# Kernel optimization log

Measured on AMD Instinct MI355X. Metric: run time of the kernel, lower is better.

The kernel has to match this reference:

```python
import jax, jax.numpy as jnp
import numpy as np

B, S, H, NH = 4, 2048, 768, 12
PH = H // NH  # per-head size


def setup_inputs() -> dict:
    key = jax.random.key(0)
    ks = jax.random.split(key, 12)
    s = 0.02
    return {
        "key": jax.random.normal(ks[0], (B, S, H), jnp.float32),
        "value": jax.random.normal(ks[1], (B, S, H), jnp.float32),
        "query": jax.random.normal(ks[2], (B, S, H), jnp.float32),
        "mask": jnp.zeros((B, 1, S, S), jnp.float32),  # additive mask
        "Wq": jax.random.normal(ks[3], (H, H), jnp.float32) * s,
        "bq": jnp.zeros((H,), jnp.float32),
        "Wk": jax.random.normal(ks[4], (H, H), jnp.float32) * s,
        "bk": jnp.zeros((H,), jnp.float32),
        "Wv": jax.random.normal(ks[5], (H, H), jnp.float32) * s,
        "bv": jnp.zeros((H,), jnp.float32),
        "Wo": jax.random.normal(ks[6], (H, H), jnp.float32) * s,
        "bo": jnp.zeros((H,), jnp.float32),
    }


def _heads(x):
    # [B,S,H] -> [B,NH,S,PH]
    return x.reshape(B, S, NH, PH).transpose(0, 2, 1, 3)


def reference(key, value, query, mask, Wq, bq, Wk, bk, Wv, bv, Wo, bo):
    # torch Linear: y = x @ W.T + b  (separate projections for q, k, v)
    q = _heads(query @ Wq.T + bq)
    k = _heads(key @ Wk.T + bk)
    v = _heads(value @ Wv.T + bv)
    scale = 1.0 / jnp.sqrt(jnp.asarray(PH, q.dtype))
    scores = jnp.einsum("bhqd,bhkd->bhqk", q, k) * scale + mask
    probs = jax.nn.softmax(scores, axis=-1)  # dropout p=0 -> identity
    out = jnp.einsum("bhqk,bhkd->bhqd", probs, v)
    out = out.transpose(0, 2, 1, 3).reshape(B, S, H)
    return out @ Wo.T + bo
```

## Files before the change

### kernel.cpp

```cpp
#include <hip/hip_runtime.h>
#include <hip/hip_bf16.h>
#include <cstddef>
#include <cstdint>

#define BB  4
#define SS  2048
#define HH  768
#define NHH 12
#define PHH 64
#define MM  (BB*SS)
#define LOG2E 1.4426950408889634f

typedef short         short8   __attribute__((ext_vector_type(8)));
typedef float         floatx4  __attribute__((ext_vector_type(4)));
typedef float         floatx16 __attribute__((ext_vector_type(16)));
typedef unsigned int  uint4v   __attribute__((ext_vector_type(4)));

static __device__ __forceinline__ unsigned short f2bf(float f) {
    unsigned int u = __float_as_uint(f);
    u += 0x7FFF + ((u >> 16) & 1);
    return (unsigned short)(u >> 16);
}

static __device__ __forceinline__ unsigned int cvtpk_bf16(float lo, float hi) {
    unsigned int r;
    asm("v_cvt_pk_bf16_f32 %0, %1, %2" : "=v"(r) : "v"(lo), "v"(hi));
    return r;
}

static __device__ __forceinline__ void plswap(unsigned int& a, unsigned int& b) {
    asm("v_permlane32_swap_b32 %0, %1" : "+v"(a), "+v"(b));
}

static __device__ __forceinline__ short8 mk_short8(unsigned int a, unsigned int b,
                                                   unsigned int c, unsigned int d) {
    uint4v u = {a, b, c, d};
    return __builtin_bit_cast(short8, u);
}

#define GLOAD_LDS16(g, l) __builtin_amdgcn_global_load_lds(            \
        (const __attribute__((address_space(1))) void*)(g),            \
        (__attribute__((address_space(3))) void*)(l), 16, 0, 0)

#define MFMA32(a, b, c) __builtin_amdgcn_mfma_f32_32x32x16_bf16((a), (b), (c), 0, 0, 0)

__global__ void mha_cvt_w4(const float* __restrict__ w0, const float* __restrict__ w1,
                           const float* __restrict__ w2, const float* __restrict__ w3,
                           unsigned short* __restrict__ dst,
                           unsigned int* __restrict__ fmask) {
    const int i = blockIdx.x * blockDim.x + threadIdx.x;
    if (blockIdx.x == 0 && threadIdx.x < 128) fmask[threadIdx.x] = 0u;
    const int which = i / 147456;
    const int j = i - which * 147456;
    const float* s = (which == 0) ? w0 : (which == 1) ? w1 : (which == 2) ? w2 : w3;
    float4 v = reinterpret_cast<const float4*>(s)[j];
    unsigned long long pk =
        (unsigned long long)f2bf(v.x)         |
        ((unsigned long long)f2bf(v.y) << 16) |
        ((unsigned long long)f2bf(v.z) << 32) |
        ((unsigned long long)f2bf(v.w) << 48);
    reinterpret_cast<unsigned long long*>(dst)[i] = pk;
}

__global__ void mha_mask_flags(const float* __restrict__ mask,
                               unsigned int* __restrict__ fmask) {
    int bid = blockIdx.x;
    int b   = bid >> 10;
    int rem = bid & 1023;
    int qt  = rem >> 5;
    int kt  = rem & 31;
    const float* base = mask + ((size_t)b*SS + (size_t)qt*64)*SS + kt*64;
    int t    = threadIdx.x;
    int lrow = t >> 4;
    int lcol = (t & 15) * 4;
    int nz = 0;
    #pragma unroll
    for (int i = 0; i < 4; ++i) {
        float4 v = *reinterpret_cast<const float4*>(base + (size_t)(lrow + 16*i)*SS + lcol);
        nz |= (v.x != 0.f) | (v.y != 0.f) | (v.z != 0.f) | (v.w != 0.f);
    }
    __shared__ int s;
    if (t == 0) s = 0;
    __syncthreads();
    if (nz) s = 1;
    __syncthreads();
    if (t == 0 && s) atomicOr(&fmask[b*32 + qt], 1u << kt);
}

template<int AIN_F32, int MODE>
__global__ __launch_bounds__(256) void mha_gemm(
        const void* __restrict__ Xv,
        const unsigned short* __restrict__ W,
        const float* __restrict__ bias,
        void* __restrict__ out) {
    __shared__ unsigned short As[64 * 32];
    __shared__ unsigned short Bs[128 * 32];
    const int wave = threadIdx.x >> 6;
    const int lane = threadIdx.x & 63;
    const int lq = lane & 15, lg = lane >> 4;
    const int m0 = blockIdx.x * 64;
    const int n0 = blockIdx.y * 128;
    const int srow = lane >> 2;
    const int scol = 8 * (lane & 3);

    const float* Xr32 = (const float*)Xv + (size_t)(m0 + wave*16 + srow)*HH + scol;
    const unsigned short* Xr16 = (const unsigned short*)Xv + (size_t)(m0 + wave*16 + srow)*HH + scol;
    const unsigned short* Wr0 = W + (size_t)(n0 + wave*32 + srow)*HH + scol;
    const unsigned short* Wr1 = W + (size_t)(n0 + wave*32 + 16 + srow)*HH + scol;
    unsigned short* As_d  = As + wave*512;
    unsigned short* As_w  = As + (wave*16 + srow)*32 + scol;
    unsigned short* Bs_d0 = Bs + wave*1024;
    unsigned short* Bs_d1 = Bs + wave*1024 + 512;

    floatx4 acc[4][2];
    #pragma unroll
    for (int m = 0; m < 4; ++m)
        #pragma unroll
        for (int n = 0; n < 2; ++n) acc[m][n] = (floatx4){0.f, 0.f, 0.f, 0.f};

    for (int k0 = 0; k0 < HH; k0 += 32) {
        if constexpr (AIN_F32) {
            float4 v0 = *reinterpret_cast<const float4*>(Xr32 + k0);
            float4 v1 = *reinterpret_cast<const float4*>(Xr32 + k0 + 4);
            GLOAD_LDS16(Wr0 + k0, Bs_d0);
            GLOAD_LDS16(Wr1 + k0, Bs_d1);
            uint4v u = { cvtpk_bf16(v0.x, v0.y), cvtpk_bf16(v0.z, v0.w),
                         cvtpk_bf16(v1.x, v1.y), cvtpk_bf16(v1.z, v1.w) };
            *reinterpret_cast<uint4v*>(As_w) = u;
        } else {
            GLOAD_LDS16(Xr16 + k0, As_d);
            GLOAD_LDS16(Wr0 + k0, Bs_d0);
            GLOAD_LDS16(Wr1 + k0, Bs_d1);
        }
        __syncthreads();
        short8 af[4], bw[2];
        #pragma unroll
        for (int m = 0; m < 4; ++m)
            af[m] = *reinterpret_cast<const short8*>(As + (16*m + lq)*32 + 8*lg);
        #pragma unroll
        for (int n = 0; n < 2; ++n)
            bw[n] = *reinterpret_cast<const short8*>(Bs + (32*wave + 16*n + lq)*32 + 8*lg);
        #pragma unroll
        for (int m = 0; m < 4; ++m)
            #pragma unroll
            for (int n = 0; n < 2; ++n)
                acc[m][n] = __builtin_amdgcn_mfma_f32_16x16x32_bf16(af[m], bw[n], acc[m][n], 0, 0, 0);
        __syncthreads();
    }

    #pragma unroll
    for (int n = 0; n < 2; ++n) {
        const int col = n0 + wave*32 + 16*n + lq;
        const float bv = bias[col];
        #pragma unroll
        for (int m = 0; m < 4; ++m) {
            #pragma unroll
            for (int r = 0; r < 4; ++r) {
                const int row = m0 + 16*m + 4*lg + r;
                float y = acc[m][n][r] + bv;
                if constexpr (MODE == 1) {
                    ((unsigned short*)out)[(size_t)row*HH + col] = f2bf(y * (0.125f * LOG2E));
                } else if constexpr (MODE == 3) {
                    ((float*)out)[(size_t)row*HH + col] = y;
                } else if constexpr (MODE == 4) {
                    int bb = row >> 11, s = row & 2047;
                    int hh = col >> 6,  d = col & 63;
                    int kt = s >> 6, half = (s >> 5) & 1, rr = s & 31;
                    int ks = d >> 4, h2 = (d >> 3) & 1, j = d & 7;
                    size_t idx = (((size_t)(bb*NHH + hh)*32 + kt)*4096)
                               + (half*4 + ks)*512 + (h2*32 + rr)*8 + j;
                    ((unsigned short*)out)[idx] = f2bf(y);
                } else {
                    int bb = row >> 11, s = row & 2047;
                    int hh = col >> 6,  d = col & 63;
                    int kt = s >> 6, ss = s & 63;
                    int ks = ss >> 4, h2 = (ss >> 3) & 1, j = ss & 7;
                    int vh = d >> 5, qq = d & 31;
                    size_t idx = (((size_t)(bb*NHH + hh)*32 + kt)*4096)
                               + (vh*4 + ks)*512 + (h2*32 + qq)*8 + j;
                    ((unsigned short*)out)[idx] = f2bf(y);
                }
            }
        }
    }
}

__global__ __launch_bounds__(256, 3) void mha_attn(
        const unsigned short* __restrict__ qb,
        const unsigned short* __restrict__ kfb,
        const unsigned short* __restrict__ vfb,
        const float* __restrict__ mask,
        const unsigned int* __restrict__ fmaskp,
        unsigned short* __restrict__ ab) {
    __shared__ unsigned short ldsbuf[2][8192];

    const int wave = threadIdx.x >> 6;
    const int lane = threadIdx.x & 63;
    const int ql   = lane & 31;
    const int hi   = lane >> 5;

    int bid = blockIdx.x;
    bid = (bid & 7) * 96 + (bid >> 3);
    const int qblk = bid & 15;
    int t = bid >> 4;
    const int h = t % NHH;
    const int b = t / NHH;

    const int q0 = qblk*128 + wave*32;
    const int q  = q0 + ql;

    const unsigned short* qp = qb + ((size_t)b*SS + q)*HH + h*PHH + 8*hi;
    short8 qf[4];
    #pragma unroll
    for (int ks = 0; ks < 4; ++ks)
        qf[ks] = *reinterpret_cast<const short8*>(qp + 16*ks);

    const unsigned short* kvK = kfb + (size_t)(b*NHH + h) * 32 * 4096;
    const unsigned short* kvV = vfb + (size_t)(b*NHH + h) * 32 * 4096;
    const float* mrow = mask + ((size_t)b*SS + q)*SS;
    const unsigned int fm = fmaskp[b*32 + (q0 >> 6)];

    float l_run = 0.f;
    floatx16 o0, o1;
    #pragma unroll
    for (int i = 0; i < 16; ++i) { o0[i] = 0.f; o1[i] = 0.f; }

#define STAGE(bufi, kti)                                                       \
    {                                                                          \
        _Pragma("unroll")                                                      \
        for (int c = 0; c < 4; ++c) {                                          \
            const int ch = 4*wave + c;                                         \
            const unsigned short* src = (ch < 8)                               \
                ? (kvK + (size_t)(kti)*4096 + ch*512)                          \
                : (kvV + (size_t)(kti)*4096 + (ch - 8)*512);                   \
            GLOAD_LDS16(src + lane*8, &ldsbuf[bufi][ch*512]);                  \
        }                                                                      \
    }

    STAGE(0, 0)

    #pragma unroll 1
    for (int kt = 0; kt < 32; ++kt) {
        const int cur = kt & 1;
        STAGE(cur ^ 1, (kt + 1) & 31)

        asm volatile("s_waitcnt vmcnt(4)" ::: "memory");
        __builtin_amdgcn_sched_barrier(0);
        __builtin_amdgcn_s_barrier();

        const unsigned short* lk = &ldsbuf[cur][0];

        short8 kf[8];
        #pragma unroll
        for (int f = 0; f < 8; ++f)
            kf[f] = *reinterpret_cast<const short8*>(lk + f*512 + lane*8);
        floatx16 s0, s1;
        #pragma unroll
        for (int i = 0; i < 16; ++i) { s0[i] = 0.f; s1[i] = 0.f; }
        __builtin_amdgcn_s_setprio(1);
        #pragma unroll
        for (int ks = 0; ks < 4; ++ks) {
            s0 = MFMA32(kf[ks],   qf[ks], s0);
            s1 = MFMA32(kf[4+ks], qf[ks], s1);
        }
        __builtin_amdgcn_s_setprio(0);

        if (fm & (1u << kt)) {
            const float* mr = mrow + kt*64;
            #pragma unroll
            for (int g = 0; g < 4; ++g) {
                float4 a = *reinterpret_cast<const float4*>(mr + 8*g + 4*hi);
                float4 c = *reinterpret_cast<const float4*>(mr + 32 + 8*g + 4*hi);
                s0[4*g+0] = fmaf(a.x, LOG2E, s0[4*g+0]);
                s0[4*g+1] = fmaf(a.y, LOG2E, s0[4*g+1]);
                s0[4*g+2] = fmaf(a.z, LOG2E, s0[4*g+2]);
                s0[4*g+3] = fmaf(a.w, LOG2E, s0[4*g+3]);
                s1[4*g+0] = fmaf(c.x, LOG2E, s1[4*g+0]);
                s1[4*g+1] = fmaf(c.y, LOG2E, s1[4*g+1]);
                s1[4*g+2] = fmaf(c.z, LOG2E, s1[4*g+2]);
                s1[4*g+3] = fmaf(c.w, LOG2E, s1[4*g+3]);
            }
        }

        float ps0 = 0.f, ps1 = 0.f, ps2 = 0.f, ps3 = 0.f;
        #pragma unroll
        for (int r = 0; r < 16; r += 4) {
            s0[r+0] = exp2f(s0[r+0]); ps0 += s0[r+0];
            s0[r+1] = exp2f(s0[r+1]); ps1 += s0[r+1];
            s0[r+2] = exp2f(s0[r+2]); ps2 += s0[r+2];
            s0[r+3] = exp2f(s0[r+3]); ps3 += s0[r+3];
        }
        #pragma unroll
        for (int r = 0; r < 16; r += 4) {
            s1[r+0] = exp2f(s1[r+0]); ps0 += s1[r+0];
            s1[r+1] = exp2f(s1[r+1]); ps1 += s1[r+1];
            s1[r+2] = exp2f(s1[r+2]); ps2 += s1[r+2];
            s1[r+3] = exp2f(s1[r+3]); ps3 += s1[r+3];
        }
        l_run += (ps0 + ps1) + (ps2 + ps3);

        unsigned int c0 = cvtpk_bf16(s0[0],  s0[1]),  c1 = cvtpk_bf16(s0[2],  s0[3]);
        unsigned int c2 = cvtpk_bf16(s0[4],  s0[5]),  c3 = cvtpk_bf16(s0[6],  s0[7]);
        unsigned int c4 = cvtpk_bf16(s0[8],  s0[9]),  c5 = cvtpk_bf16(s0[10], s0[11]);
        unsigned int c6 = cvtpk_bf16(s0[12], s0[13]), c7 = cvtpk_bf16(s0[14], s0[15]);
        unsigned int d0 = cvtpk_bf16(s1[0],  s1[1]),  d1 = cvtpk_bf16(s1[2],  s1[3]);
        unsigned int d2 = cvtpk_bf16(s1[4],  s1[5]),  d3 = cvtpk_bf16(s1[6],  s1[7]);
        unsigned int d4 = cvtpk_bf16(s1[8],  s1[9]),  d5 = cvtpk_bf16(s1[10], s1[11]);
        unsigned int d6 = cvtpk_bf16(s1[12], s1[13]), d7 = cvtpk_bf16(s1[14], s1[15]);
        plswap(c0, c2); plswap(c1, c3); plswap(c4, c6); plswap(c5, c7);
        plswap(d0, d2); plswap(d1, d3); plswap(d4, d6); plswap(d5, d7);
        short8 pa[4];
        pa[0] = mk_short8(c0, c1, c2, c3);
        pa[1] = mk_short8(c4, c5, c6, c7);
        pa[2] = mk_short8(d0, d1, d2, d3);
        pa[3] = mk_short8(d4, d5, d6, d7);

        const unsigned short* lv = lk + 4096;
        short8 vf[8];
        #pragma unroll
        for (int g = 0; g < 8; ++g)
            vf[g] = *reinterpret_cast<const short8*>(lv + g*512 + lane*8);
        __builtin_amdgcn_s_setprio(1);
        #pragma unroll
        for (int ks = 0; ks < 4; ++ks) {
            o0 = MFMA32(vf[ks],   pa[ks], o0);
            o1 = MFMA32(vf[4+ks], pa[ks], o1);
        }
        __builtin_amdgcn_s_setprio(0);

        asm volatile("s_waitcnt lgkmcnt(0)" ::: "memory");
        __builtin_amdgcn_sched_barrier(0);
        __builtin_amdgcn_s_barrier();
    }
#undef STAGE

    const float l_tot = l_run + __shfl_xor(l_run, 32);
    const float inv = 1.f / l_tot;
    unsigned short* op = ab + ((size_t)b*SS + q)*HH + h*PHH + 4*hi;
    #pragma unroll
    for (int g = 0; g < 4; ++g) {
        ushort4 w0, w1;
        w0.x = f2bf(o0[4*g+0]*inv); w0.y = f2bf(o0[4*g+1]*inv);
        w0.z = f2bf(o0[4*g+2]*inv); w0.w = f2bf(o0[4*g+3]*inv);
        w1.x = f2bf(o1[4*g+0]*inv); w1.y = f2bf(o1[4*g+1]*inv);
        w1.z = f2bf(o1[4*g+2]*inv); w1.w = f2bf(o1[4*g+3]*inv);
        *reinterpret_cast<ushort4*>(op + 8*g)      = w0;
        *reinterpret_cast<ushort4*>(op + 32 + 8*g) = w1;
    }
}

extern "C" void kernel_launch(void* const* d_in, const int* in_sizes, int n_in,
                              void* d_out, int out_size, void* d_ws, size_t ws_size,
                              hipStream_t stream) {
    const float* key   = (const float*)d_in[0];
    const float* value = (const float*)d_in[1];
    const float* query = (const float*)d_in[2];
    const float* mask  = (const float*)d_in[3];
    const float* Wq    = (const float*)d_in[4];
    const float* bq    = (const float*)d_in[5];
    const float* Wk    = (const float*)d_in[6];
    const float* bk    = (const float*)d_in[7];
    const float* Wv    = (const float*)d_in[8];
    const float* bv    = (const float*)d_in[9];
    const float* Wo    = (const float*)d_in[10];
    const float* bo    = (const float*)d_in[11];
    float* out = (float*)d_out;

    const size_t WSZ = (size_t)HH * HH;
    const size_t ASZ = (size_t)MM * HH;
    unsigned short* wqb = (unsigned short*)d_ws;
    unsigned short* wkb = wqb + WSZ;
    unsigned short* wvb = wkb + WSZ;
    unsigned short* wob = wvb + WSZ;
    unsigned short* qb  = wob + WSZ;
    unsigned short* kfb = qb + ASZ;
    unsigned short* vfb = kfb + ASZ;
    unsigned short* xb  = vfb + ASZ;
    unsigned int* fmask = (unsigned int*)(xb + ASZ);

    mha_cvt_w4<<<(4*147456)/256, 256, 0, stream>>>(Wq, Wk, Wv, Wo, wqb, fmask);

    mha_mask_flags<<<BB*32*32, 256, 0, stream>>>(mask, fmask);

    dim3 g(MM/64, HH/128);
    mha_gemm<1,1><<<g, 256, 0, stream>>>(query, wqb, bq, qb);
    mha_gemm<1,4><<<g, 256, 0, stream>>>(key,   wkb, bk, kfb);
    mha_gemm<1,5><<<g, 256, 0, stream>>>(value, wvb, bv, vfb);

    mha_attn<<<BB*NHH*(SS/128), 256, 0, stream>>>(qb, kfb, vfb, mask, fmask, xb);

    mha_gemm<0,3><<<g, 256, 0, stream>>>(xb, wob, bo, out);
}
```

Baseline: 189.9 us.

## Batch QKV projections into one launch, compute softmax row sums via MFMA

The three Q/K/V projection GEMMs are merged into a single launch with a z grid dimension that selects the input, weight, bias and output layout per block. This removes two launches and lets the three projections run concurrently on the GPU. In the attention kernel the per-lane exp2 sums are replaced by an extra MFMA against a ones vector, which accumulates the softmax denominator on the matrix unit and drops the final cross-lane shuffle. exp2f is also swapped for the raw v_exp_f32 instruction. The extra MFMA adds matrix-unit work per tile, the row sums are now taken from bf16-rounded probabilities, and the z-dependent branches in the epilogue add some divergence-free overhead.

```diff
diff --git a/kernel.cpp b/kernel.cpp
--- a/kernel.cpp
+++ b/kernel.cpp
@@ -25,6 +25,12 @@
 static __device__ __forceinline__ unsigned int cvtpk_bf16(float lo, float hi) {
     unsigned int r;
     asm("v_cvt_pk_bf16_f32 %0, %1, %2" : "=v"(r) : "v"(lo), "v"(hi));
+    return r;
+}
+
+static __device__ __forceinline__ float v_exp2(float x) {
+    float r;
+    asm("v_exp_f32 %0, %1" : "=v"(r) : "v"(x));
     return r;
 }
 
@@ -87,12 +93,117 @@
     if (t == 0 && s) atomicOr(&fmask[b*32 + qt], 1u << kt);
 }
 
-template<int AIN_F32, int MODE>
-__global__ __launch_bounds__(256) void mha_gemm(
-        const void* __restrict__ Xv,
+struct GemmCtx {
+    const float* Xr32; const unsigned short* Wr0; const unsigned short* Wr1;
+    unsigned short *As_w, *Bs_d0, *Bs_d1;
+    const unsigned short* As; const unsigned short* Bs;
+    int wave, lq, lg;
+};
+
+__device__ __forceinline__ void gemm_body(const GemmCtx& c, floatx4 (&acc)[4][2]) {
+    #pragma unroll
+    for (int m = 0; m < 4; ++m)
+        #pragma unroll
+        for (int n = 0; n < 2; ++n) acc[m][n] = (floatx4){0.f, 0.f, 0.f, 0.f};
+    for (int k0 = 0; k0 < HH; k0 += 32) {
+        float4 v0 = *reinterpret_cast<const float4*>(c.Xr32 + k0);
+        float4 v1 = *reinterpret_cast<const float4*>(c.Xr32 + k0 + 4);
+        GLOAD_LDS16(c.Wr0 + k0, c.Bs_d0);
+        GLOAD_LDS16(c.Wr1 + k0, c.Bs_d1);
+        uint4v u = { cvtpk_bf16(v0.x, v0.y), cvtpk_bf16(v0.z, v0.w),
+                     cvtpk_bf16(v1.x, v1.y), cvtpk_bf16(v1.z, v1.w) };
+        *reinterpret_cast<uint4v*>(c.As_w) = u;
+        __syncthreads();
+        short8 af[4], bw[2];
+        #pragma unroll
+        for (int m = 0; m < 4; ++m)
+            af[m] = *reinterpret_cast<const short8*>(c.As + (16*m + c.lq)*32 + 8*c.lg);
+        #pragma unroll
+        for (int n = 0; n < 2; ++n)
+            bw[n] = *reinterpret_cast<const short8*>(c.Bs + (32*c.wave + 16*n + c.lq)*32 + 8*c.lg);
+        #pragma unroll
+        for (int m = 0; m < 4; ++m)
+            #pragma unroll
+            for (int n = 0; n < 2; ++n)
+                acc[m][n] = __builtin_amdgcn_mfma_f32_16x16x32_bf16(af[m], bw[n], acc[m][n], 0, 0, 0);
+        __syncthreads();
+    }
+}
+
+__global__ __launch_bounds__(256) void mha_gemm_qkv(
+        const float* __restrict__ qx, const float* __restrict__ kx,
+        const float* __restrict__ vx,
+        const unsigned short* __restrict__ wq, const unsigned short* __restrict__ wk,
+        const unsigned short* __restrict__ wv,
+        const float* __restrict__ bqp, const float* __restrict__ bkp,
+        const float* __restrict__ bvp,
+        unsigned short* __restrict__ qb, unsigned short* __restrict__ kfb,
+        unsigned short* __restrict__ vfb) {
+    __shared__ unsigned short As[64 * 32];
+    __shared__ unsigned short Bs[128 * 32];
+    const int z = blockIdx.z;
+    const float* X = (z == 0) ? qx : (z == 1) ? kx : vx;
+    const unsigned short* W = (z == 0) ? wq : (z == 1) ? wk : wv;
+    const float* bias = (z == 0) ? bqp : (z == 1) ? bkp : bvp;
+
+    const int wave = threadIdx.x >> 6;
+    const int lane = threadIdx.x & 63;
+    const int lq = lane & 15, lg = lane >> 4;
+    const int m0 = blockIdx.x * 64;
+    const int n0 = blockIdx.y * 128;
+    const int srow = lane >> 2;
+    const int scol = 8 * (lane & 3);
+
+    GemmCtx c;
+    c.Xr32 = X + (size_t)(m0 + wave*16 + srow)*HH + scol;
+    c.Wr0  = W + (size_t)(n0 + wave*32 + srow)*HH + scol;
+    c.Wr1  = W + (size_t)(n0 + wave*32 + 16 + srow)*HH + scol;
+    c.As_w = As + (wave*16 + srow)*32 + scol;
+    c.Bs_d0 = Bs + wave*1024;
+    c.Bs_d1 = Bs + wave*1024 + 512;
+    c.As = As; c.Bs = Bs; c.wave = wave; c.lq = lq; c.lg = lg;
+
+    floatx4 acc[4][2];
+    gemm_body(c, acc);
+
+    #pragma unroll
+    for (int n = 0; n < 2; ++n) {
+        const int col = n0 + wave*32 + 16*n + lq;
+        const float bv = bias[col];
+        #pragma unroll
+        for (int m = 0; m < 4; ++m) {
+            #pragma unroll
+            for (int r = 0; r < 4; ++r) {
+                const int row = m0 + 16*m + 4*lg + r;
+                float y = acc[m][n][r] + bv;
+                int bb = row >> 11, s = row & 2047;
+                int hh = col >> 6,  d = col & 63;
+                if (z == 0) {
+                    qb[(size_t)row*HH + col] = f2bf(y * (0.125f * LOG2E));
+                } else if (z == 1) {
+                    int kt = s >> 6, half = (s >> 5) & 1, rr = s & 31;
+                    int ks = d >> 4, h2 = (d >> 3) & 1, j = d & 7;
+                    size_t idx = (((size_t)(bb*NHH + hh)*32 + kt)*4096)
+                               + (half*4 + ks)*512 + (h2*32 + rr)*8 + j;
+                    kfb[idx] = f2bf(y);
+                } else {
+                    int kt = s >> 6, ss = s & 63;
+                    int ks = ss >> 4, h2 = (ss >> 3) & 1, j = ss & 7;
+                    int vh = d >> 5, qq = d & 31;
+                    size_t idx = (((size_t)(bb*NHH + hh)*32 + kt)*4096)
+                               + (vh*4 + ks)*512 + (h2*32 + qq)*8 + j;
+                    vfb[idx] = f2bf(y);
+                }
+            }
+        }
+    }
+}
+
+__global__ __launch_bounds__(256) void mha_gemm_out(
+        const unsigned short* __restrict__ X,
         const unsigned short* __restrict__ W,
         const float* __restrict__ bias,
-        void* __restrict__ out) {
+        float* __restrict__ out) {
     __shared__ unsigned short As[64 * 32];
     __shared__ unsigned short Bs[128 * 32];
     const int wave = threadIdx.x >> 6;
@@ -103,12 +214,10 @@
     const int srow = lane >> 2;
     const int scol = 8 * (lane & 3);
 
-    const float* Xr32 = (const float*)Xv + (size_t)(m0 + wave*16 + srow)*HH + scol;
-    const unsigned short* Xr16 = (const unsigned short*)Xv + (size_t)(m0 + wave*16 + srow)*HH + scol;
+    const unsigned short* Xr16 = X + (size_t)(m0 + wave*16 + srow)*HH + scol;
     const unsigned short* Wr0 = W + (size_t)(n0 + wave*32 + srow)*HH + scol;
     const unsigned short* Wr1 = W + (size_t)(n0 + wave*32 + 16 + srow)*HH + scol;
     unsigned short* As_d  = As + wave*512;
-    unsigned short* As_w  = As + (wave*16 + srow)*32 + scol;
     unsigned short* Bs_d0 = Bs + wave*1024;
     unsigned short* Bs_d1 = Bs + wave*1024 + 512;
 
@@ -119,19 +228,9 @@
         for (int n = 0; n < 2; ++n) acc[m][n] = (floatx4){0.f, 0.f, 0.f, 0.f};
 
     for (int k0 = 0; k0 < HH; k0 += 32) {
-        if constexpr (AIN_F32) {
-            float4 v0 = *reinterpret_cast<const float4*>(Xr32 + k0);
-            float4 v1 = *reinterpret_cast<const float4*>(Xr32 + k0 + 4);
-            GLOAD_LDS16(Wr0 + k0, Bs_d0);
-            GLOAD_LDS16(Wr1 + k0, Bs_d1);
-            uint4v u = { cvtpk_bf16(v0.x, v0.y), cvtpk_bf16(v0.z, v0.w),
-                         cvtpk_bf16(v1.x, v1.y), cvtpk_bf16(v1.z, v1.w) };
-            *reinterpret_cast<uint4v*>(As_w) = u;
-        } else {
-            GLOAD_LDS16(Xr16 + k0, As_d);
-            GLOAD_LDS16(Wr0 + k0, Bs_d0);
-            GLOAD_LDS16(Wr1 + k0, Bs_d1);
-        }
+        GLOAD_LDS16(Xr16 + k0, As_d);
+        GLOAD_LDS16(Wr0 + k0, Bs_d0);
+        GLOAD_LDS16(Wr1 + k0, Bs_d1);
         __syncthreads();
         short8 af[4], bw[2];
         #pragma unroll
@@ -153,35 +252,10 @@
         const int col = n0 + wave*32 + 16*n + lq;
         const float bv = bias[col];
         #pragma unroll
-        for (int m = 0; m < 4; ++m) {
+        for (int m = 0; m < 4; ++m)
             #pragma unroll
-            for (int r = 0; r < 4; ++r) {
-                const int row = m0 + 16*m + 4*lg + r;
-                float y = acc[m][n][r] + bv;
-                if constexpr (MODE == 1) {
-                    ((unsigned short*)out)[(size_t)row*HH + col] = f2bf(y * (0.125f * LOG2E));
-                } else if constexpr (MODE == 3) {
-                    ((float*)out)[(size_t)row*HH + col] = y;
-                } else if constexpr (MODE == 4) {
-                    int bb = row >> 11, s = row & 2047;
-                    int hh = col >> 6,  d = col & 63;
-                    int kt = s >> 6, half = (s >> 5) & 1, rr = s & 31;
-                    int ks = d >> 4, h2 = (d >> 3) & 1, j = d & 7;
-                    size_t idx = (((size_t)(bb*NHH + hh)*32 + kt)*4096)
-                               + (half*4 + ks)*512 + (h2*32 + rr)*8 + j;
-                    ((unsigned short*)out)[idx] = f2bf(y);
-                } else {
-                    int bb = row >> 11, s = row & 2047;
-                    int hh = col >> 6,  d = col & 63;
-                    int kt = s >> 6, ss = s & 63;
-                    int ks = ss >> 4, h2 = (ss >> 3) & 1, j = ss & 7;
-                    int vh = d >> 5, qq = d & 31;
-                    size_t idx = (((size_t)(bb*NHH + hh)*32 + kt)*4096)
-                               + (vh*4 + ks)*512 + (h2*32 + qq)*8 + j;
-                    ((unsigned short*)out)[idx] = f2bf(y);
-                }
-            }
-        }
+            for (int r = 0; r < 4; ++r)
+                out[(size_t)(m0 + 16*m + 4*lg + r)*HH + col] = acc[m][n][r] + bv;
     }
 }
 
@@ -215,15 +289,18 @@
     for (int ks = 0; ks < 4; ++ks)
         qf[ks] = *reinterpret_cast<const short8*>(qp + 16*ks);
 
+    short8 ones;
+    #pragma unroll
+    for (int i = 0; i < 8; ++i) ones[i] = (short)0x3F80;
+
     const unsigned short* kvK = kfb + (size_t)(b*NHH + h) * 32 * 4096;
     const unsigned short* kvV = vfb + (size_t)(b*NHH + h) * 32 * 4096;
     const float* mrow = mask + ((size_t)b*SS + q)*SS;
     const unsigned int fm = fmaskp[b*32 + (q0 >> 6)];
 
-    float l_run = 0.f;
-    floatx16 o0, o1;
-    #pragma unroll
-    for (int i = 0; i < 16; ++i) { o0[i] = 0.f; o1[i] = 0.f; }
+    floatx16 o0, o1, lacc;
+    #pragma unroll
+    for (int i = 0; i < 16; ++i) { o0[i] = 0.f; o1[i] = 0.f; lacc[i] = 0.f; }
 
 #define STAGE(bufi, kti)                                                       \
     {                                                                          \
@@ -282,22 +359,10 @@
             }
         }
 
-        float ps0 = 0.f, ps1 = 0.f, ps2 = 0.f, ps3 = 0.f;
-        #pragma unroll
-        for (int r = 0; r < 16; r += 4) {
-            s0[r+0] = exp2f(s0[r+0]); ps0 += s0[r+0];
-            s0[r+1] = exp2f(s0[r+1]); ps1 += s0[r+1];
-            s0[r+2] = exp2f(s0[r+2]); ps2 += s0[r+2];
-            s0[r+3] = exp2f(s0[r+3]); ps3 += s0[r+3];
-        }
-        #pragma unroll
-        for (int r = 0; r < 16; r += 4) {
-            s1[r+0] = exp2f(s1[r+0]); ps0 += s1[r+0];
-            s1[r+1] = exp2f(s1[r+1]); ps1 += s1[r+1];
-            s1[r+2] = exp2f(s1[r+2]); ps2 += s1[r+2];
-            s1[r+3] = exp2f(s1[r+3]); ps3 += s1[r+3];
-        }
-        l_run += (ps0 + ps1) + (ps2 + ps3);
+        #pragma unroll
+        for (int r = 0; r < 16; ++r) s0[r] = v_exp2(s0[r]);
+        #pragma unroll
+        for (int r = 0; r < 16; ++r) s1[r] = v_exp2(s1[r]);
 
         unsigned int c0 = cvtpk_bf16(s0[0],  s0[1]),  c1 = cvtpk_bf16(s0[2],  s0[3]);
         unsigned int c2 = cvtpk_bf16(s0[4],  s0[5]),  c3 = cvtpk_bf16(s0[6],  s0[7]);
@@ -323,8 +388,9 @@
         __builtin_amdgcn_s_setprio(1);
         #pragma unroll
         for (int ks = 0; ks < 4; ++ks) {
-            o0 = MFMA32(vf[ks],   pa[ks], o0);
-            o1 = MFMA32(vf[4+ks], pa[ks], o1);
+            o0   = MFMA32(vf[ks],   pa[ks], o0);
+            o1   = MFMA32(vf[4+ks], pa[ks], o1);
+            lacc = MFMA32(ones,     pa[ks], lacc);
         }
         __builtin_amdgcn_s_setprio(0);
 
@@ -334,8 +400,7 @@
     }
 #undef STAGE
 
-    const float l_tot = l_run + __shfl_xor(l_run, 32);
-    const float inv = 1.f / l_tot;
+    const float inv = 1.f / lacc[0];
     unsigned short* op = ab + ((size_t)b*SS + q)*HH + h*PHH + 4*hi;
     #pragma unroll
     for (int g = 0; g < 4; ++g) {
@@ -382,12 +447,13 @@
 
     mha_mask_flags<<<BB*32*32, 256, 0, stream>>>(mask, fmask);
 
+    dim3 g3(MM/64, HH/128, 3);
+    mha_gemm_qkv<<<g3, 256, 0, stream>>>(query, key, value,
+                                         wqb, wkb, wvb, bq, bk, bv,
+                                         qb, kfb, vfb);
+
+    mha_attn<<<BB*NHH*(SS/128), 256, 0, stream>>>(qb, kfb, vfb, mask, fmask, xb);
+
     dim3 g(MM/64, HH/128);
-    mha_gemm<1,1><<<g, 256, 0, stream>>>(query, wqb, bq, qb);
-    mha_gemm<1,4><<<g, 256, 0, stream>>>(key,   wkb, bk, kfb);
-    mha_gemm<1,5><<<g, 256, 0, stream>>>(value, wvb, bv, vfb);
-
-    mha_attn<<<BB*NHH*(SS/128), 256, 0, stream>>>(qb, kfb, vfb, mask, fmask, xb);
-
-    mha_gemm<0,3><<<g, 256, 0, stream>>>(xb, wob, bo, out);
-}
+    mha_gemm_out<<<g, 256, 0, stream>>>(xb, wob, bo, out);
+}
```

Result: faster. 171.4 us (-9.7%).
